# Kernel tuning notes

Hardware: AMD Instinct MI355X
Metric: run time of the kernel (lower is better)

The kernel has to match this reference:

```python
import jax, jax.numpy as jnp
import numpy as np

N = 4096        # num nodes == input_dim (required: [N,N] scores += [N,input_dim] dng)
D_IN = 4096
D_MODEL = 1024
K_W = 10        # num_weights
LN_EPS = 1e-5   # torch LayerNorm default


def setup_inputs() -> dict:
    key = jax.random.key(0)
    ks = jax.random.split(key, 16)
    s = 0.02  # small init so softmax over the [N,N] biased scores stays well-conditioned
    return {
        "x": jax.random.normal(ks[0], (N, D_IN), jnp.float32) * s,
        "adjacency_matrix": (jax.random.uniform(ks[1], (N, N)) < 0.01).astype(jnp.float32),
        "graph_metrics": jax.random.normal(ks[2], (N, N), jnp.float32) * s,
        "weights": jax.random.uniform(ks[3], (N, K_W), jnp.float32),
        "W_stack": jax.random.normal(ks[4], (K_W, D_IN, D_MODEL), jnp.float32) * s,
        "b_stack": jnp.zeros((K_W, D_MODEL), jnp.float32),
        "Wq": jax.random.normal(ks[5], (D_MODEL, D_MODEL), jnp.float32) * s,
        "bq": jnp.zeros((D_MODEL,), jnp.float32),
        "Wk": jax.random.normal(ks[6], (D_MODEL, D_MODEL), jnp.float32) * s,
        "bk": jnp.zeros((D_MODEL,), jnp.float32),
        "Wv": jax.random.normal(ks[7], (D_MODEL, D_MODEL), jnp.float32) * s,
        "bv": jnp.zeros((D_MODEL,), jnp.float32),
        "Wo": jax.random.normal(ks[8], (D_MODEL, D_IN), jnp.float32) * s,
        "bo": jnp.zeros((D_IN,), jnp.float32),
        "gamma": jnp.ones((D_MODEL,), jnp.float32),
        "beta": jnp.zeros((D_MODEL,), jnp.float32),
    }


def _layer_norm(h, gamma, beta):
    mu = jnp.mean(h, axis=-1, keepdims=True)
    var = jnp.mean(jnp.square(h - mu), axis=-1, keepdims=True)
    return (h - mu) * jax.lax.rsqrt(var + LN_EPS) * gamma + beta


def reference(x, adjacency_matrix, graph_metrics, weights,
              W_stack, b_stack, Wq, bq, Wk, bk, Wv, bv, Wo, bo, gamma, beta):
    A = adjacency_matrix  # [N,N] float
    # --- graph-derived additive bias (dng_scores) ---
    direct = A @ x                                   # [N, D_IN]
    inter = A @ A                                    # [N, N]
    row = jnp.sum(A, axis=1, keepdims=True)          # [N, 1]
    col = jnp.sum(A, axis=0, keepdims=True)          # [1, N]
    sim = inter / (row + col - inter + 1e-6)         # neighborhood similarity [N,N]
    dng = direct + sim @ x + graph_metrics @ x       # [N, D_IN] (== [N, N])
    # --- weighted input projection (apply_weights, vectorized over K_W linears) ---
    weighted_x = jnp.einsum('ni,kio,nk->no', x, W_stack, weights) + weights @ b_stack
    h = _layer_norm(weighted_x, gamma, beta)         # [N, D_MODEL]
    # --- single-head attention with additive dng bias ---
    Q = h @ Wq + bq
    K = h @ Wk + bk
    V = h @ Wv + bv
    scores = Q @ K.T / np.sqrt(D_MODEL).astype(np.float32) + dng  # [N, N]
    attn = jax.nn.softmax(scores, axis=-1)
    out = attn @ V                                   # [N, D_MODEL]
    y = out @ Wo + bo                                # [N, D_IN]; dropout is eval-mode identity
    return jax.nn.relu(y + dng)
```

## Files before the change

### kernel.cpp

```cpp
#include <hip/hip_runtime.h>
#include <hip/hip_bf16.h>

typedef unsigned short u16;
typedef __bf16 bf16x8 __attribute__((ext_vector_type(8)));
typedef float f32x4 __attribute__((ext_vector_type(4)));

__device__ __forceinline__ u16 f2bf(float v) {
    __hip_bfloat16 h = __float2bfloat16(v);
    return __builtin_bit_cast(u16, h);
}
__device__ __forceinline__ float bf2f(u16 v) {
    __hip_bfloat16 h = __builtin_bit_cast(__hip_bfloat16, v);
    return __bfloat162float(h);
}

__device__ __forceinline__ void gld_lds16(const u16* g, u16* l) {
    __builtin_amdgcn_global_load_lds(
        (const __attribute__((address_space(1))) unsigned int*)(const void*)g,
        (__attribute__((address_space(3))) unsigned int*)(void*)l, 16, 0, 0);
}


__global__ void k_convert_bf16(const float* __restrict__ s, u16* __restrict__ d, long n) {
    long i = ((long)blockIdx.x * 256 + threadIdx.x) * 4;
    if (i < n) {
        float4 v = *(const float4*)(s + i);
        u16 a = f2bf(v.x), b = f2bf(v.y), c = f2bf(v.z), e = f2bf(v.w);
        ushort4 o; o.x = a; o.y = b; o.z = c; o.w = e;
        *(ushort4*)(d + i) = o;
    }
}

__global__ void k_zero_f32(float* __restrict__ p) {
    float4 z; z.x = z.y = z.z = z.w = 0.f;
    ((float4*)p)[(size_t)blockIdx.x * 256 + threadIdx.x] = z;
}

__global__ void k_transpose_f32_bf16(const float* __restrict__ src, u16* __restrict__ dst,
                                     int R, int C, int ld_src, int ld_dst) {
    __shared__ u16 t[32][33];
    int c0 = blockIdx.x * 32, r0 = blockIdx.y * 32;
    int tx = threadIdx.x & 31, ty = threadIdx.x >> 5;
#pragma unroll
    for (int i = 0; i < 32; i += 8)
        t[ty + i][tx] = f2bf(src[(size_t)(r0 + ty + i) * ld_src + c0 + tx]);
    __syncthreads();
#pragma unroll
    for (int i = 0; i < 32; i += 8)
        dst[(size_t)(c0 + ty + i) * ld_dst + r0 + tx] = t[tx][ty + i];
}

__global__ void k_transpose_u16(const u16* __restrict__ src, u16* __restrict__ dst,
                                int R, int C, int ld_src, int ld_dst) {
    __shared__ u16 t[32][33];
    int c0 = blockIdx.x * 32, r0 = blockIdx.y * 32;
    int tx = threadIdx.x & 31, ty = threadIdx.x >> 5;
#pragma unroll
    for (int i = 0; i < 32; i += 8)
        t[ty + i][tx] = src[(size_t)(r0 + ty + i) * ld_src + c0 + tx];
    __syncthreads();
#pragma unroll
    for (int i = 0; i < 32; i += 8)
        dst[(size_t)(c0 + ty + i) * ld_dst + r0 + tx] = t[tx][ty + i];
}

__global__ void k_rowsum(const float* __restrict__ A, float* __restrict__ r) {
    __shared__ float sm[4];
    const float4* p = (const float4*)(A + (size_t)blockIdx.x * 4096);
    float s = 0.f;
#pragma unroll
    for (int j = 0; j < 4; ++j) {
        float4 v = p[threadIdx.x + j * 256];
        s += v.x + v.y + v.z + v.w;
    }
#pragma unroll
    for (int o = 32; o; o >>= 1) s += __shfl_down(s, o, 64);
    if ((threadIdx.x & 63) == 0) sm[threadIdx.x >> 6] = s;
    __syncthreads();
    if (threadIdx.x == 0) r[blockIdx.x] = sm[0] + sm[1] + sm[2] + sm[3];
}

__global__ void k_rowsum_bf16(const u16* __restrict__ A, float* __restrict__ r) {
    __shared__ float sm[4];
    const ushort4* p = (const ushort4*)(A + (size_t)blockIdx.x * 4096);
    float s = 0.f;
#pragma unroll
    for (int j = 0; j < 4; ++j) {
        ushort4 v = p[threadIdx.x + j * 256];
        s += bf2f(v.x) + bf2f(v.y) + bf2f(v.z) + bf2f(v.w);
    }
#pragma unroll
    for (int o = 32; o; o >>= 1) s += __shfl_down(s, o, 64);
    if ((threadIdx.x & 63) == 0) sm[threadIdx.x >> 6] = s;
    __syncthreads();
    if (threadIdx.x == 0) r[blockIdx.x] = sm[0] + sm[1] + sm[2] + sm[3];
}

__global__ void k_bias_concat(const float* __restrict__ bq, const float* __restrict__ bk,
                              const float* __restrict__ bv, float* __restrict__ o) {
    int i = blockIdx.x * 256 + threadIdx.x;
    o[i] = i < 1024 ? bq[i] : (i < 2048 ? bk[i - 1024] : bv[i - 2048]);
}

__global__ void k_layernorm(const float* __restrict__ wx, const float* __restrict__ gamma,
                            const float* __restrict__ beta, u16* __restrict__ h) {
    __shared__ float sm[8];
    size_t base = (size_t)blockIdx.x * 1024;
    float4 v = ((const float4*)(wx + base))[threadIdx.x];
    float s = v.x + v.y + v.z + v.w;
    float q = v.x * v.x + v.y * v.y + v.z * v.z + v.w * v.w;
#pragma unroll
    for (int o = 32; o; o >>= 1) { s += __shfl_down(s, o, 64); q += __shfl_down(q, o, 64); }
    int lane = threadIdx.x & 63, w = threadIdx.x >> 6;
    if (lane == 0) { sm[w] = s; sm[4 + w] = q; }
    __syncthreads();
    s = sm[0] + sm[1] + sm[2] + sm[3];
    q = sm[4] + sm[5] + sm[6] + sm[7];
    float mu = s * (1.f / 1024.f);
    float var = q * (1.f / 1024.f) - mu * mu;
    float rstd = rsqrtf(var + 1e-5f);
    int c = threadIdx.x * 4;
    ushort4 o;
    o.x = f2bf((v.x - mu) * rstd * gamma[c + 0] + beta[c + 0]);
    o.y = f2bf((v.y - mu) * rstd * gamma[c + 1] + beta[c + 1]);
    o.z = f2bf((v.z - mu) * rstd * gamma[c + 2] + beta[c + 2]);
    o.w = f2bf((v.w - mu) * rstd * gamma[c + 3] + beta[c + 3]);
    *(ushort4*)(h + base + c) = o;
}

__global__ void k_softmax(const float* __restrict__ S, u16* __restrict__ P) {
    __shared__ float sm[8];
    size_t base = (size_t)blockIdx.x * 4096;
    const float4* p = (const float4*)(S + base);
    float4 v[4];
#pragma unroll
    for (int j = 0; j < 4; ++j) v[j] = p[threadIdx.x + j * 256];
    float m = -3.4e38f;
#pragma unroll
    for (int j = 0; j < 4; ++j)
        m = fmaxf(m, fmaxf(fmaxf(v[j].x, v[j].y), fmaxf(v[j].z, v[j].w)));
#pragma unroll
    for (int o = 32; o; o >>= 1) m = fmaxf(m, __shfl_down(m, o, 64));
    int lane = threadIdx.x & 63, w = threadIdx.x >> 6;
    if (lane == 0) sm[w] = m;
    __syncthreads();
    m = fmaxf(fmaxf(sm[0], sm[1]), fmaxf(sm[2], sm[3]));
    float s = 0.f;
#pragma unroll
    for (int j = 0; j < 4; ++j) {
        v[j].x = __expf(v[j].x - m); v[j].y = __expf(v[j].y - m);
        v[j].z = __expf(v[j].z - m); v[j].w = __expf(v[j].w - m);
        s += v[j].x + v[j].y + v[j].z + v[j].w;
    }
#pragma unroll
    for (int o = 32; o; o >>= 1) s += __shfl_down(s, o, 64);
    if (lane == 0) sm[4 + w] = s;
    __syncthreads();
    s = sm[4] + sm[5] + sm[6] + sm[7];
    float inv = 1.f / s;
#pragma unroll
    for (int j = 0; j < 4; ++j) {
        ushort4 o;
        o.x = f2bf(v[j].x * inv); o.y = f2bf(v[j].y * inv);
        o.z = f2bf(v[j].z * inv); o.w = f2bf(v[j].w * inv);
        *(ushort4*)(P + base + (size_t)(threadIdx.x + j * 256) * 4) = o;
    }
}


#define EPI_M_BUILD 0
#define EPI_F32     1
#define EPI_WEIGHTED 2
#define EPI_QKV     3
#define EPI_SCORES  4
#define EPI_BF16    5
#define EPI_FINAL   6

template <int EPI>
__launch_bounds__(256, 2)
__global__ void gemm_bt(const u16* __restrict__ A, const u16* __restrict__ Bt,
                        int K, int lda, int ldb, int ldc,
                        void* __restrict__ Cout,
                        const float* __restrict__ e0, const float* __restrict__ e1,
                        const float* __restrict__ e2, const float* __restrict__ e3,
                        float scale, int kidx, size_t zb) {
    __shared__ __align__(16) u16 As[128 * 32];
    __shared__ __align__(16) u16 Bs[128 * 32];
    const int tid = threadIdx.x;
    const int m0 = blockIdx.y * 128, n0 = blockIdx.x * 128;
    const int lane = tid & 63, wave = tid >> 6;
    const int wm = (wave >> 1) * 64, wn = (wave & 1) * 64;
    const int fr = lane & 15, quad = lane >> 4;

    Bt += (size_t)blockIdx.z * zb;

    f32x4 acc[4][4] = {};

    const int ar = tid >> 2, ak = (tid & 3) * 8;
    const u16* gA0 = A + (size_t)(m0 + ar) * lda + ak;
    const u16* gA1 = gA0 + (size_t)64 * lda;
    const u16* gB0 = Bt + (size_t)(n0 + ar) * ldb + ak;
    const u16* gB1 = gB0 + (size_t)64 * ldb;
    u16* lA0 = As + tid * 8;
    u16* lA1 = As + (tid + 256) * 8;
    u16* lB0 = Bs + tid * 8;
    u16* lB1 = Bs + (tid + 256) * 8;

    for (int kk = 0; kk < K; kk += 32) {
        __syncthreads();
        gld_lds16(gA0 + kk, lA0);
        gld_lds16(gA1 + kk, lA1);
        gld_lds16(gB0 + kk, lB0);
        gld_lds16(gB1 + kk, lB1);
        __syncthreads();

        bf16x8 af[4], bfv[4];
#pragma unroll
        for (int i = 0; i < 4; ++i)
            af[i] = *(const bf16x8*)(As + (wm + i * 16 + fr) * 32 + quad * 8);
#pragma unroll
        for (int i = 0; i < 4; ++i)
            bfv[i] = *(const bf16x8*)(Bs + (wn + i * 16 + fr) * 32 + quad * 8);
#pragma unroll
        for (int mi = 0; mi < 4; ++mi)
#pragma unroll
            for (int ni = 0; ni < 4; ++ni)
                acc[mi][ni] = __builtin_amdgcn_mfma_f32_16x16x32_bf16(af[mi], bfv[ni], acc[mi][ni], 0, 0, 0);
    }

#pragma unroll
    for (int mi = 0; mi < 4; ++mi) {
#pragma unroll
        for (int r = 0; r < 4; ++r) {
            int row = m0 + wm + mi * 16 + quad * 4 + r;
#pragma unroll
            for (int ni = 0; ni < 4; ++ni) {
                int col = n0 + wn + ni * 16 + fr;
                float v = acc[mi][ni][r];
                size_t ci = (size_t)row * ldc + col;
                if constexpr (EPI == EPI_M_BUILD) {
                    size_t gi = (size_t)row * 4096 + col;
                    float denom = e2[row] + e3[col] - v + 1e-6f;
                    ((u16*)Cout)[ci] = f2bf(e0[gi] + v / denom + e1[gi]);
                } else if constexpr (EPI == EPI_F32) {
                    ((float*)Cout)[ci] = v;
                } else if constexpr (EPI == EPI_WEIGHTED) {
                    float w = e0[(size_t)row * 10 + blockIdx.z];
                    atomicAdd((float*)Cout + ci,
                              w * (v + e1[(size_t)blockIdx.z * 1024 + col]));
                } else if constexpr (EPI == EPI_QKV) {
                    ((u16*)Cout)[ci] = f2bf(v + e0[col]);
                } else if constexpr (EPI == EPI_SCORES) {
                    ((float*)Cout)[ci] = v * scale + e0[(size_t)row * 4096 + col];
                } else if constexpr (EPI == EPI_BF16) {
                    ((u16*)Cout)[ci] = f2bf(v);
                } else {
                    float y = v + e0[col] + e1[(size_t)row * 4096 + col];
                    ((float*)Cout)[ci] = y > 0.f ? y : 0.f;
                }
            }
        }
    }
}


extern "C" void kernel_launch(void* const* d_in, const int* in_sizes, int n_in,
                              void* d_out, int out_size, void* d_ws, size_t ws_size,
                              hipStream_t stream) {
    (void)in_sizes; (void)n_in; (void)out_size; (void)ws_size;
    const float* x   = (const float*)d_in[0];
    const float* A   = (const float*)d_in[1];
    const float* gm  = (const float*)d_in[2];
    const float* wts = (const float*)d_in[3];
    const float* Wst = (const float*)d_in[4];
    const float* bst = (const float*)d_in[5];
    const float* Wq  = (const float*)d_in[6];
    const float* bq  = (const float*)d_in[7];
    const float* Wk  = (const float*)d_in[8];
    const float* bk  = (const float*)d_in[9];
    const float* Wv  = (const float*)d_in[10];
    const float* bv  = (const float*)d_in[11];
    const float* Wo  = (const float*)d_in[12];
    const float* bo  = (const float*)d_in[13];
    const float* gamma = (const float*)d_in[14];
    const float* beta  = (const float*)d_in[15];
    float* out = (float*)d_out;
    char* ws = (char*)d_ws;

    const int N = 4096, DM = 1024;
    const size_t MB32 = 33554432UL;
    u16*   A_bf   = (u16*)(ws + 0);
    u16*   A_bfT  = (u16*)(ws + MB32);
    float* scores = (float*)(ws + 0);
    u16*   x_bfT  = (u16*)(ws + 2 * MB32);
    u16*   attn   = (u16*)(ws + 2 * MB32);
    u16*   x_bf   = (u16*)(ws + 3 * MB32);
    u16*   WqkvT  = (u16*)(ws + 3 * MB32);
    float* bqkv   = (float*)(ws + 3 * MB32 + 6291456UL);
    u16*   QKV    = (u16*)(ws + 3 * MB32 + 6307840UL);
    u16*   M_bf   = (u16*)(ws + 4 * MB32);
    u16*   WallT  = (u16*)(ws + 0);
    u16*   V_T    = (u16*)(ws + 4 * MB32);
    u16*   WoT    = (u16*)(ws + 4 * MB32 + 8388608UL);
    u16*   out_bf = (u16*)(ws + 4 * MB32 + 16777216UL);
    float* dng    = (float*)(ws + 5 * MB32);
    float* wxf    = (float*)(ws + 5 * MB32 + 67108864UL);
    u16*   h_bf   = (u16*)(ws + 5 * MB32 + 83886080UL);
    float* rowS   = (float*)(ws + 5 * MB32 + 92274688UL);
    float* colS   = (float*)(ws + 5 * MB32 + 92291072UL);

    k_convert_bf16<<<16384, 256, 0, stream>>>(A, A_bf, (long)N * N);
    k_transpose_f32_bf16<<<dim3(128, 128), 256, 0, stream>>>(A, A_bfT, N, N, N, N);
    k_convert_bf16<<<16384, 256, 0, stream>>>(x, x_bf, (long)N * N);
    k_transpose_f32_bf16<<<dim3(128, 128), 256, 0, stream>>>(x, x_bfT, N, N, N, N);
    k_rowsum<<<N, 256, 0, stream>>>(A, rowS);
    k_rowsum_bf16<<<N, 256, 0, stream>>>(A_bfT, colS);

    gemm_bt<EPI_M_BUILD><<<dim3(32, 32), 256, 0, stream>>>(
        A_bf, A_bfT, N, N, N, N, M_bf, A, gm, rowS, colS, 0.f, 0, 0);

    gemm_bt<EPI_F32><<<dim3(32, 32), 256, 0, stream>>>(
        M_bf, x_bfT, N, N, N, N, dng, nullptr, nullptr, nullptr, nullptr, 0.f, 0, 0);

    for (int k = 0; k < 10; ++k)
        k_transpose_f32_bf16<<<dim3(32, 128), 256, 0, stream>>>(
            Wst + (size_t)k * N * DM, WallT + (size_t)k * DM * N, N, DM, DM, N);
    k_zero_f32<<<4096, 256, 0, stream>>>(wxf);
    gemm_bt<EPI_WEIGHTED><<<dim3(8, 32, 10), 256, 0, stream>>>(
        x_bf, WallT, N, N, N, DM, wxf, wts, bst, nullptr, nullptr, 0.f, 0, (size_t)DM * N);

    k_transpose_f32_bf16<<<dim3(32, 32), 256, 0, stream>>>(Wq, WqkvT, DM, DM, DM, DM);
    k_transpose_f32_bf16<<<dim3(32, 32), 256, 0, stream>>>(Wk, WqkvT + (size_t)DM * DM, DM, DM, DM, DM);
    k_transpose_f32_bf16<<<dim3(32, 32), 256, 0, stream>>>(Wv, WqkvT + 2 * (size_t)DM * DM, DM, DM, DM, DM);
    k_bias_concat<<<12, 256, 0, stream>>>(bq, bk, bv, bqkv);
    k_layernorm<<<N, 256, 0, stream>>>(wxf, gamma, beta, h_bf);

    gemm_bt<EPI_QKV><<<dim3(24, 32), 256, 0, stream>>>(
        h_bf, WqkvT, DM, DM, DM, 3072, QKV, bqkv, nullptr, nullptr, nullptr, 0.f, 0, 0);

    k_transpose_u16<<<dim3(32, 128), 256, 0, stream>>>(QKV + 2048, V_T, N, DM, 3072, N);

    gemm_bt<EPI_SCORES><<<dim3(32, 32), 256, 0, stream>>>(
        QKV, QKV + 1024, DM, 3072, 3072, N, scores, dng, nullptr, nullptr, nullptr, 0.03125f, 0, 0);

    k_softmax<<<N, 256, 0, stream>>>(scores, attn);

    gemm_bt<EPI_BF16><<<dim3(8, 32), 256, 0, stream>>>(
        attn, V_T, N, N, N, DM, out_bf, nullptr, nullptr, nullptr, nullptr, 0.f, 0, 0);

    k_transpose_f32_bf16<<<dim3(128, 32), 256, 0, stream>>>(Wo, WoT, DM, N, N, DM);
    gemm_bt<EPI_FINAL><<<dim3(32, 32), 256, 0, stream>>>(
        out_bf, WoT, DM, DM, DM, N, out, bo, dng, nullptr, nullptr, 0.f, 0, 0);
}
```

Measured before the change: 1.507 ms.

## Replace atomic weighted-projection accumulation with register-accumulated two-way split GEMM

The weighted input projection previously launched 10 z-slices that each atomically added into a zeroed fp32 buffer. It is now a dedicated GEMM where each block loops over 5 of the weight matrices and accumulates the weighted results in registers. It writes plain stores to one of two partial buffers, which layernorm sums on load. This removes the zero-fill kernel and the atomic traffic, but cuts grid parallelism from 2560 to 512 blocks and adds a second accumulator array, raising register pressure.

```diff
diff --git a/kernel.cpp b/kernel.cpp
--- a/kernel.cpp
+++ b/kernel.cpp
@@ -31,11 +31,6 @@
     }
 }
 
-__global__ void k_zero_f32(float* __restrict__ p) {
-    float4 z; z.x = z.y = z.z = z.w = 0.f;
-    ((float4*)p)[(size_t)blockIdx.x * 256 + threadIdx.x] = z;
-}
-
 __global__ void k_transpose_f32_bf16(const float* __restrict__ src, u16* __restrict__ dst,
                                      int R, int C, int ld_src, int ld_dst) {
     __shared__ u16 t[32][33];
@@ -102,11 +97,15 @@
     o[i] = i < 1024 ? bq[i] : (i < 2048 ? bk[i - 1024] : bv[i - 2048]);
 }
 
-__global__ void k_layernorm(const float* __restrict__ wx, const float* __restrict__ gamma,
+__global__ void k_layernorm(const float* __restrict__ wx0, const float* __restrict__ wx1,
+                            const float* __restrict__ gamma,
                             const float* __restrict__ beta, u16* __restrict__ h) {
     __shared__ float sm[8];
     size_t base = (size_t)blockIdx.x * 1024;
-    float4 v = ((const float4*)(wx + base))[threadIdx.x];
+    float4 a = ((const float4*)(wx0 + base))[threadIdx.x];
+    float4 b = ((const float4*)(wx1 + base))[threadIdx.x];
+    float4 v;
+    v.x = a.x + b.x; v.y = a.y + b.y; v.z = a.z + b.z; v.w = a.w + b.w;
     float s = v.x + v.y + v.z + v.w;
     float q = v.x * v.x + v.y * v.y + v.z * v.z + v.w * v.w;
 #pragma unroll
@@ -170,7 +169,6 @@
 
 #define EPI_M_BUILD 0
 #define EPI_F32     1
-#define EPI_WEIGHTED 2
 #define EPI_QKV     3
 #define EPI_SCORES  4
 #define EPI_BF16    5
@@ -244,10 +242,6 @@
                     ((u16*)Cout)[ci] = f2bf(e0[gi] + v / denom + e1[gi]);
                 } else if constexpr (EPI == EPI_F32) {
                     ((float*)Cout)[ci] = v;
-                } else if constexpr (EPI == EPI_WEIGHTED) {
-                    float w = e0[(size_t)row * 10 + blockIdx.z];
-                    atomicAdd((float*)Cout + ci,
-                              w * (v + e1[(size_t)blockIdx.z * 1024 + col]));
                 } else if constexpr (EPI == EPI_QKV) {
                     ((u16*)Cout)[ci] = f2bf(v + e0[col]);
                 } else if constexpr (EPI == EPI_SCORES) {
@@ -258,6 +252,90 @@
                     float y = v + e0[col] + e1[(size_t)row * 4096 + col];
                     ((float*)Cout)[ci] = y > 0.f ? y : 0.f;
                 }
+            }
+        }
+    }
+}
+
+
+__launch_bounds__(256, 2)
+__global__ void gemm_wsum(const u16* __restrict__ A, const u16* __restrict__ Bt,
+                          const float* __restrict__ wts, const float* __restrict__ bst,
+                          float* __restrict__ C0, float* __restrict__ C1) {
+    __shared__ __align__(16) u16 As[128 * 32];
+    __shared__ __align__(16) u16 Bs[128 * 32];
+    const int tid = threadIdx.x;
+    const int m0 = blockIdx.y * 128, n0 = blockIdx.x * 128;
+    const int lane = tid & 63, wave = tid >> 6;
+    const int wm = (wave >> 1) * 64, wn = (wave & 1) * 64;
+    const int fr = lane & 15, quad = lane >> 4;
+    const int k0 = blockIdx.z * 5;
+
+    const int ar = tid >> 2, ak = (tid & 3) * 8;
+    const u16* gA0 = A + (size_t)(m0 + ar) * 4096 + ak;
+    const u16* gA1 = gA0 + (size_t)64 * 4096;
+    u16* lA0 = As + tid * 8;
+    u16* lA1 = As + (tid + 256) * 8;
+    u16* lB0 = Bs + tid * 8;
+    u16* lB1 = Bs + (tid + 256) * 8;
+
+    f32x4 acc[4][4] = {};
+
+    for (int s = 0; s < 5; ++s) {
+        const int k = k0 + s;
+        const u16* gB0 = Bt + (size_t)k * 1024 * 4096 + (size_t)(n0 + ar) * 4096 + ak;
+        const u16* gB1 = gB0 + (size_t)64 * 4096;
+
+        f32x4 acck[4][4] = {};
+        for (int kk = 0; kk < 4096; kk += 32) {
+            __syncthreads();
+            gld_lds16(gA0 + kk, lA0);
+            gld_lds16(gA1 + kk, lA1);
+            gld_lds16(gB0 + kk, lB0);
+            gld_lds16(gB1 + kk, lB1);
+            __syncthreads();
+
+            bf16x8 af[4], bfv[4];
+#pragma unroll
+            for (int i = 0; i < 4; ++i)
+                af[i] = *(const bf16x8*)(As + (wm + i * 16 + fr) * 32 + quad * 8);
+#pragma unroll
+            for (int i = 0; i < 4; ++i)
+                bfv[i] = *(const bf16x8*)(Bs + (wn + i * 16 + fr) * 32 + quad * 8);
+#pragma unroll
+            for (int mi = 0; mi < 4; ++mi)
+#pragma unroll
+                for (int ni = 0; ni < 4; ++ni)
+                    acck[mi][ni] = __builtin_amdgcn_mfma_f32_16x16x32_bf16(af[mi], bfv[ni], acck[mi][ni], 0, 0, 0);
+        }
+
+        float bv[4];
+#pragma unroll
+        for (int ni = 0; ni < 4; ++ni)
+            bv[ni] = bst[(size_t)k * 1024 + n0 + wn + ni * 16 + fr];
+#pragma unroll
+        for (int mi = 0; mi < 4; ++mi) {
+#pragma unroll
+            for (int r = 0; r < 4; ++r) {
+                int row = m0 + wm + mi * 16 + quad * 4 + r;
+                float w = wts[(size_t)row * 10 + k];
+#pragma unroll
+                for (int ni = 0; ni < 4; ++ni)
+                    acc[mi][ni][r] += w * (acck[mi][ni][r] + bv[ni]);
+            }
+        }
+    }
+
+    float* Cout = blockIdx.z ? C1 : C0;
+#pragma unroll
+    for (int mi = 0; mi < 4; ++mi) {
+#pragma unroll
+        for (int r = 0; r < 4; ++r) {
+            int row = m0 + wm + mi * 16 + quad * 4 + r;
+#pragma unroll
+            for (int ni = 0; ni < 4; ++ni) {
+                int col = n0 + wn + ni * 16 + fr;
+                Cout[(size_t)row * 1024 + col] = acc[mi][ni][r];
             }
         }
     }
@@ -299,6 +377,7 @@
     float* bqkv   = (float*)(ws + 3 * MB32 + 6291456UL);
     u16*   QKV    = (u16*)(ws + 3 * MB32 + 6307840UL);
     u16*   M_bf   = (u16*)(ws + 4 * MB32);
+    float* wxf2   = (float*)(ws + 4 * MB32);
     u16*   WallT  = (u16*)(ws + 0);
     u16*   V_T    = (u16*)(ws + 4 * MB32);
     u16*   WoT    = (u16*)(ws + 4 * MB32 + 8388608UL);
@@ -325,15 +404,13 @@
     for (int k = 0; k < 10; ++k)
         k_transpose_f32_bf16<<<dim3(32, 128), 256, 0, stream>>>(
             Wst + (size_t)k * N * DM, WallT + (size_t)k * DM * N, N, DM, DM, N);
-    k_zero_f32<<<4096, 256, 0, stream>>>(wxf);
-    gemm_bt<EPI_WEIGHTED><<<dim3(8, 32, 10), 256, 0, stream>>>(
-        x_bf, WallT, N, N, N, DM, wxf, wts, bst, nullptr, nullptr, 0.f, 0, (size_t)DM * N);
+    gemm_wsum<<<dim3(8, 32, 2), 256, 0, stream>>>(x_bf, WallT, wts, bst, wxf, wxf2);
 
     k_transpose_f32_bf16<<<dim3(32, 32), 256, 0, stream>>>(Wq, WqkvT, DM, DM, DM, DM);
     k_transpose_f32_bf16<<<dim3(32, 32), 256, 0, stream>>>(Wk, WqkvT + (size_t)DM * DM, DM, DM, DM, DM);
     k_transpose_f32_bf16<<<dim3(32, 32), 256, 0, stream>>>(Wv, WqkvT + 2 * (size_t)DM * DM, DM, DM, DM, DM);
     k_bias_concat<<<12, 256, 0, stream>>>(bq, bk, bv, bqkv);
-    k_layernorm<<<N, 256, 0, stream>>>(wxf, gamma, beta, h_bf);
+    k_layernorm<<<N, 256, 0, stream>>>(wxf, wxf2, gamma, beta, h_bf);
 
     gemm_bt<EPI_QKV><<<dim3(24, 32), 256, 0, stream>>>(
         h_bf, WqkvT, DM, DM, DM, 3072, QKV, bqkv, nullptr, nullptr, nullptr, 0.f, 0, 0);
```

Result: no change. 1.505 ms (-0.1%).

## Add 256x256 eight-wave pipelined GEMM with swizzled LDS and double buffering

Applied to the files above, without the earlier changes.

Introduces a new 512-thread GEMM kernel with 256x256 output tiles and 64-wide K steps. It double-buffers direct global-to-LDS loads with XOR-swizzled addressing, staggers load issue across four MFMA phases separated by barriers, raises wave priority with setprio, and remaps workgroups with a block swizzle. All GEMMs except attn@V move to it, and the weighted projection becomes a single N=10240 GEMM with column-derived weight indexing. The aim is more data reuse per tile and memory latency hidden behind MFMA work. The cost is higher LDS use (128KB per block) and fewer blocks in flight.

```diff
diff --git a/kernel.cpp b/kernel.cpp
--- a/kernel.cpp
+++ b/kernel.cpp
@@ -167,7 +167,6 @@
     }
 }
 
-
 #define EPI_M_BUILD 0
 #define EPI_F32     1
 #define EPI_WEIGHTED 2
@@ -175,6 +174,7 @@
 #define EPI_SCORES  4
 #define EPI_BF16    5
 #define EPI_FINAL   6
+
 
 template <int EPI>
 __launch_bounds__(256, 2)
@@ -238,29 +238,138 @@
                 int col = n0 + wn + ni * 16 + fr;
                 float v = acc[mi][ni][r];
                 size_t ci = (size_t)row * ldc + col;
-                if constexpr (EPI == EPI_M_BUILD) {
-                    size_t gi = (size_t)row * 4096 + col;
-                    float denom = e2[row] + e3[col] - v + 1e-6f;
-                    ((u16*)Cout)[ci] = f2bf(e0[gi] + v / denom + e1[gi]);
+                if constexpr (EPI == EPI_BF16) {
+                    ((u16*)Cout)[ci] = f2bf(v);
                 } else if constexpr (EPI == EPI_F32) {
                     ((float*)Cout)[ci] = v;
-                } else if constexpr (EPI == EPI_WEIGHTED) {
-                    float w = e0[(size_t)row * 10 + blockIdx.z];
-                    atomicAdd((float*)Cout + ci,
-                              w * (v + e1[(size_t)blockIdx.z * 1024 + col]));
-                } else if constexpr (EPI == EPI_QKV) {
-                    ((u16*)Cout)[ci] = f2bf(v + e0[col]);
-                } else if constexpr (EPI == EPI_SCORES) {
-                    ((float*)Cout)[ci] = v * scale + e0[(size_t)row * 4096 + col];
-                } else if constexpr (EPI == EPI_BF16) {
-                    ((u16*)Cout)[ci] = f2bf(v);
-                } else {
-                    float y = v + e0[col] + e1[(size_t)row * 4096 + col];
-                    ((float*)Cout)[ci] = y > 0.f ? y : 0.f;
                 }
             }
         }
     }
+}
+
+
+#define FENCE() asm volatile("" ::: "memory")
+#define BAR8() { FENCE(); __builtin_amdgcn_s_barrier(); FENCE(); }
+
+template <int EPI>
+__launch_bounds__(512, 2)
+__global__ void gemm8(const u16* __restrict__ Ag, const u16* __restrict__ Bt,
+                      int K, int lda, int ldb, int ldc, void* __restrict__ Cout,
+                      const float* __restrict__ e0, const float* __restrict__ e1,
+                      const float* __restrict__ e2, const float* __restrict__ e3,
+                      float scale) {
+    __shared__ __align__(16) u16 S[65536];
+    const int tid = threadIdx.x;
+    const int bid = blockIdx.y * gridDim.x + blockIdx.x;
+    const int nwg = gridDim.x * gridDim.y;
+    const int swz = (bid & 7) * (nwg >> 3) + (bid >> 3);
+    const int m0 = (swz / gridDim.x) * 256;
+    const int n0 = (swz % gridDim.x) * 256;
+
+    const int srow = tid >> 3;
+    const int skc8 = ((tid & 7) ^ (srow & 7)) * 8;
+    const u16* gA = Ag + (size_t)(m0 + srow) * lda + skc8;
+    const u16* gB = Bt + (size_t)(n0 + srow) * ldb + skc8;
+    u16* dst = S + tid * 8;
+
+    const int lane = tid & 63, wave = tid >> 6;
+    const int wn = (wave & 3) * 64;
+    const int wmA = (wave >> 2) * 64;
+    const int fr = lane & 15, quad = lane >> 4;
+    const int kc0 = (quad ^ (fr & 7)) * 8;
+    const int kc1 = ((quad ^ (fr & 7)) ^ 4) * 8;
+
+#define ISSUE_A(b, s, kk) { \
+    gld_lds16(gA + (size_t)((s) * 64) * lda + (kk), dst + (b) * 32768 + (s) * 8192); \
+    gld_lds16(gA + (size_t)((s) * 64 + 128) * lda + (kk), dst + (b) * 32768 + (s) * 8192 + 4096); }
+#define ISSUE_B(b, s, kk) { \
+    gld_lds16(gB + (size_t)((s) * 128) * ldb + (kk), dst + (b) * 32768 + 16384 + (s) * 8192); \
+    gld_lds16(gB + (size_t)((s) * 128 + 64) * ldb + (kk), dst + (b) * 32768 + 16384 + (s) * 8192 + 4096); }
+
+    ISSUE_A(0, 0, 0); ISSUE_B(0, 0, 0); ISSUE_B(0, 1, 0); ISSUE_A(0, 1, 0);
+    ISSUE_A(1, 0, 64); ISSUE_B(1, 0, 64); ISSUE_B(1, 1, 64);
+
+    f32x4 acc[8][4] = {};
+    const int NT = K >> 6;
+
+#define AR8(q, f, ks) (*(const bf16x8*)(SA + (((q) >> 1) * 128 + wmA + ((q) & 1) * 32 + (f) * 16 + fr) * 64 + ((ks) ? kc1 : kc0)))
+#define PHASE(q) { \
+    bf16x8 a00 = AR8(q, 0, 0), a01 = AR8(q, 0, 1), a10 = AR8(q, 1, 0), a11 = AR8(q, 1, 1); \
+    __builtin_amdgcn_s_setprio(1); \
+    _Pragma("unroll") \
+    for (int fn = 0; fn < 4; ++fn) { \
+        acc[2 * (q)][fn]     = __builtin_amdgcn_mfma_f32_16x16x32_bf16(a00, bfr[fn][0], acc[2 * (q)][fn], 0, 0, 0); \
+        acc[2 * (q) + 1][fn] = __builtin_amdgcn_mfma_f32_16x16x32_bf16(a10, bfr[fn][0], acc[2 * (q) + 1][fn], 0, 0, 0); \
+    } \
+    _Pragma("unroll") \
+    for (int fn = 0; fn < 4; ++fn) { \
+        acc[2 * (q)][fn]     = __builtin_amdgcn_mfma_f32_16x16x32_bf16(a01, bfr[fn][1], acc[2 * (q)][fn], 0, 0, 0); \
+        acc[2 * (q) + 1][fn] = __builtin_amdgcn_mfma_f32_16x16x32_bf16(a11, bfr[fn][1], acc[2 * (q) + 1][fn], 0, 0, 0); \
+    } \
+    __builtin_amdgcn_s_setprio(0); \
+    asm volatile("s_waitcnt lgkmcnt(0)" ::: "memory"); }
+
+    for (int t = 0; t < NT; ++t) {
+        const int b = t & 1;
+        const u16* SA = S + b * 32768;
+        const u16* SB = SA + 16384;
+        if (t + 1 < NT) ISSUE_A(b ^ 1, 1, (t + 1) * 64);
+        if (t < NT - 1) { asm volatile("s_waitcnt vmcnt(8)" ::: "memory"); }
+        else            { asm volatile("s_waitcnt vmcnt(0)" ::: "memory"); }
+        BAR8();
+        bf16x8 bfr[4][2];
+#pragma unroll
+        for (int fn = 0; fn < 4; ++fn) {
+            bfr[fn][0] = *(const bf16x8*)(SB + (wn + fn * 16 + fr) * 64 + kc0);
+            bfr[fn][1] = *(const bf16x8*)(SB + (wn + fn * 16 + fr) * 64 + kc1);
+        }
+        PHASE(0);
+        BAR8();
+        PHASE(1);
+        BAR8();
+        if (t + 2 < NT) ISSUE_A(b, 0, (t + 2) * 64);
+        PHASE(2);
+        BAR8();
+        if (t + 2 < NT) { ISSUE_B(b, 0, (t + 2) * 64); ISSUE_B(b, 1, (t + 2) * 64); }
+        PHASE(3);
+        BAR8();
+    }
+
+    const int wmC = (wave >> 2) * 128;
+#pragma unroll
+    for (int fm = 0; fm < 8; ++fm) {
+#pragma unroll
+        for (int r = 0; r < 4; ++r) {
+            const int row = m0 + wmC + fm * 16 + quad * 4 + r;
+#pragma unroll
+            for (int fn = 0; fn < 4; ++fn) {
+                const int col = n0 + wn + fn * 16 + fr;
+                float vv = acc[fm][fn][r];
+                if constexpr (EPI == EPI_M_BUILD) {
+                    size_t gi = (size_t)row * 4096 + col;
+                    float denom = e2[row] + e3[col] - vv + 1e-6f;
+                    ((u16*)Cout)[gi] = f2bf(e0[gi] + vv / denom + e1[gi]);
+                } else if constexpr (EPI == EPI_F32) {
+                    ((float*)Cout)[(size_t)row * ldc + col] = vv;
+                } else if constexpr (EPI == EPI_WEIGHTED) {
+                    atomicAdd((float*)Cout + (size_t)row * 1024 + (col & 1023),
+                              e0[(size_t)row * 10 + (col >> 10)] * (vv + e1[col]));
+                } else if constexpr (EPI == EPI_QKV) {
+                    ((u16*)Cout)[(size_t)row * ldc + col] = f2bf(vv + e0[col]);
+                } else if constexpr (EPI == EPI_SCORES) {
+                    ((float*)Cout)[(size_t)row * ldc + col] = vv * scale + e0[(size_t)row * 4096 + col];
+                } else {
+                    float y = vv + e0[col] + e1[(size_t)row * 4096 + col];
+                    ((float*)Cout)[(size_t)row * ldc + col] = y > 0.f ? y : 0.f;
+                }
+            }
+        }
+    }
+#undef ISSUE_A
+#undef ISSUE_B
+#undef AR8
+#undef PHASE
 }
 
 
@@ -316,18 +425,18 @@
     k_rowsum<<<N, 256, 0, stream>>>(A, rowS);
     k_rowsum_bf16<<<N, 256, 0, stream>>>(A_bfT, colS);
 
-    gemm_bt<EPI_M_BUILD><<<dim3(32, 32), 256, 0, stream>>>(
-        A_bf, A_bfT, N, N, N, N, M_bf, A, gm, rowS, colS, 0.f, 0, 0);
-
-    gemm_bt<EPI_F32><<<dim3(32, 32), 256, 0, stream>>>(
-        M_bf, x_bfT, N, N, N, N, dng, nullptr, nullptr, nullptr, nullptr, 0.f, 0, 0);
+    gemm8<EPI_M_BUILD><<<dim3(16, 16), 512, 0, stream>>>(
+        A_bf, A_bfT, N, N, N, N, M_bf, A, gm, rowS, colS, 0.f);
+
+    gemm8<EPI_F32><<<dim3(16, 16), 512, 0, stream>>>(
+        M_bf, x_bfT, N, N, N, N, dng, nullptr, nullptr, nullptr, nullptr, 0.f);
 
     for (int k = 0; k < 10; ++k)
         k_transpose_f32_bf16<<<dim3(32, 128), 256, 0, stream>>>(
             Wst + (size_t)k * N * DM, WallT + (size_t)k * DM * N, N, DM, DM, N);
     k_zero_f32<<<4096, 256, 0, stream>>>(wxf);
-    gemm_bt<EPI_WEIGHTED><<<dim3(8, 32, 10), 256, 0, stream>>>(
-        x_bf, WallT, N, N, N, DM, wxf, wts, bst, nullptr, nullptr, 0.f, 0, (size_t)DM * N);
+    gemm8<EPI_WEIGHTED><<<dim3(40, 16), 512, 0, stream>>>(
+        x_bf, WallT, N, N, N, DM, wxf, wts, bst, nullptr, nullptr, 0.f);
 
     k_transpose_f32_bf16<<<dim3(32, 32), 256, 0, stream>>>(Wq, WqkvT, DM, DM, DM, DM);
     k_transpose_f32_bf16<<<dim3(32, 32), 256, 0, stream>>>(Wk, WqkvT + (size_t)DM * DM, DM, DM, DM, DM);
@@ -335,13 +444,13 @@
     k_bias_concat<<<12, 256, 0, stream>>>(bq, bk, bv, bqkv);
     k_layernorm<<<N, 256, 0, stream>>>(wxf, gamma, beta, h_bf);
 
-    gemm_bt<EPI_QKV><<<dim3(24, 32), 256, 0, stream>>>(
-        h_bf, WqkvT, DM, DM, DM, 3072, QKV, bqkv, nullptr, nullptr, nullptr, 0.f, 0, 0);
+    gemm8<EPI_QKV><<<dim3(12, 16), 512, 0, stream>>>(
+        h_bf, WqkvT, DM, DM, DM, 3072, QKV, bqkv, nullptr, nullptr, nullptr, 0.f);
 
     k_transpose_u16<<<dim3(32, 128), 256, 0, stream>>>(QKV + 2048, V_T, N, DM, 3072, N);
 
-    gemm_bt<EPI_SCORES><<<dim3(32, 32), 256, 0, stream>>>(
-        QKV, QKV + 1024, DM, 3072, 3072, N, scores, dng, nullptr, nullptr, nullptr, 0.03125f, 0, 0);
+    gemm8<EPI_SCORES><<<dim3(16, 16), 512, 0, stream>>>(
+        QKV, QKV + 1024, DM, 3072, 3072, N, scores, dng, nullptr, nullptr, nullptr, 0.03125f);
 
     k_softmax<<<N, 256, 0, stream>>>(scores, attn);
 
@@ -349,6 +458,6 @@
         attn, V_T, N, N, N, DM, out_bf, nullptr, nullptr, nullptr, nullptr, 0.f, 0, 0);
 
     k_transpose_f32_bf16<<<dim3(128, 32), 256, 0, stream>>>(Wo, WoT, DM, N, N, DM);
-    gemm_bt<EPI_FINAL><<<dim3(32, 32), 256, 0, stream>>>(
-        out_bf, WoT, DM, DM, DM, N, out, bo, dng, nullptr, nullptr, 0.f, 0, 0);
-}
+    gemm8<EPI_FINAL><<<dim3(16, 16), 512, 0, stream>>>(
+        out_bf, WoT, DM, DM, DM, N, out, bo, dng, nullptr, nullptr, 0.f);
+}
```

Result: faster. 1.392 ms (-7.6%).
